# Kernel tuning notes

Measured on AMD Instinct MI355X. Metric: run time of the kernel, lower is better.

The kernel has to match this reference:

```python
import jax, jax.numpy as jnp
import numpy as np

D_MODEL = 256
D_INNER = 512
D_STATE = 16
DT_RANK = 16
D_CONV = 4


def setup_inputs() -> dict:
    key = jax.random.key(0)
    ks = jax.random.split(key, 10)
    f32 = jnp.float32
    x = jax.random.normal(ks[0], (8, D_MODEL, 128, 128), dtype=f32)
    W_in = jax.random.normal(ks[1], (D_MODEL, 2 * D_INNER), dtype=f32) * 0.02
    conv_w = jax.random.normal(ks[2], (D_INNER, D_CONV), dtype=f32) * 0.1
    conv_b = jnp.zeros((D_INNER,), dtype=f32)
    W_xproj = jax.random.normal(ks[3], (D_INNER, DT_RANK + 2 * D_STATE), dtype=f32) * 0.02
    W_dt = jax.random.normal(ks[4], (DT_RANK, D_INNER), dtype=f32) * 0.1
    b_dt = jax.random.normal(ks[5], (D_INNER,), dtype=f32) * 0.1
    # S4D-real init used by Mamba: A = -[1..d_state]
    A_log = jnp.log(jnp.broadcast_to(
        jnp.arange(1, D_STATE + 1, dtype=f32), (D_INNER, D_STATE))).copy()
    D = jnp.ones((D_INNER,), dtype=f32)
    W_out = jax.random.normal(ks[6], (D_INNER, D_MODEL), dtype=f32) * 0.02
    return {"x": x, "W_in": W_in, "conv_w": conv_w, "conv_b": conv_b,
            "W_xproj": W_xproj, "W_dt": W_dt, "b_dt": b_dt,
            "A_log": A_log, "D": D, "W_out": W_out}


def _mamba_l1(u, W_in, conv_w, conv_b, W_xproj, W_dt, b_dt, A_log, D, W_out):
    """Mamba block on N independent length-1 sequences. u: [N, d_model]."""
    dt_rank = W_dt.shape[0]
    d_state = A_log.shape[1]
    xz = u @ W_in                                   # [N, 2*d_inner]
    xi, z = jnp.split(xz, 2, axis=-1)               # each [N, d_inner]
    # Causal depthwise conv with left zero-padding; for L=1 only the last tap fires.
    xc = jax.nn.silu(xi * conv_w[:, -1] + conv_b)   # [N, d_inner]
    dbc = xc @ W_xproj                              # [N, dt_rank + 2*d_state]
    dt = dbc[:, :dt_rank]
    Bm = dbc[:, dt_rank:dt_rank + d_state]          # [N, d_state]
    Cm = dbc[:, dt_rank + d_state:]                 # [N, d_state]
    delta = jax.nn.softplus(dt @ W_dt + b_dt)       # [N, d_inner]
    # Single scan step from h0 = 0:
    #   h = exp(delta*A)*h0 + delta*B*u = delta*B*u  (A_log has zero effect/grad)
    #   y_d = sum_s h_{d,s} * C_s + D_d * u_d = delta_d*u_d*(B.C) + D_d*u_d
    bc = jnp.sum(Bm * Cm, axis=-1, keepdims=True)   # [N, 1]
    y = delta * xc * bc + D * xc                    # [N, d_inner]
    y = y * jax.nn.silu(z)
    return y @ W_out                                # [N, d_model]


def reference(x, W_in, conv_w, conv_b, W_xproj, W_dt, b_dt, A_log, D, W_out):
    B_, C, H, W = x.shape
    xs = x.transpose(0, 2, 3, 1).reshape(-1, C)     # [N, d_model], N = B*H*W
    y1 = _mamba_l1(xs, W_in, conv_w, conv_b, W_xproj, W_dt, b_dt, A_log, D, W_out)
    # torch.flip over a length-1 sequence dim is the identity -> y2 == y1
    y = (y1 + y1) * 0.5
    return y.reshape(B_, H, W, C).transpose(0, 3, 1, 2)
```

## Files before the change

kernel.cpp:

```cpp
#include <hip/hip_runtime.h>


typedef _Float16 f16x8 __attribute__((ext_vector_type(8)));
typedef _Float16 f16x2 __attribute__((ext_vector_type(2)));
typedef __fp16 fp16x2b __attribute__((ext_vector_type(2)));
typedef float f32x4 __attribute__((ext_vector_type(4)));

#define MFMA16(a,b,c) __builtin_amdgcn_mfma_f32_16x16x32_f16((a),(b),(c),0,0,0)

#define WPIN_OFF   0u
#define WPOUT_OFF  524288u
#define WPXP_OFF   786432u
#define WPDT_OFF   835584u

#define U_OFF     0
#define XC_OFF    0
#define DTP_OFF   65536
#define BC_OFF    69632
#define LDS_BYTES 69888

__device__ __forceinline__ unsigned short f16bits(float f) {
  union { _Float16 h; unsigned short u; } c; c.h = (_Float16)f; return c.u;
}
__device__ __forceinline__ unsigned pk2(float a, float b) {
  union { fp16x2b h; unsigned u; } c;
  c.h = __builtin_amdgcn_cvt_pkrtz(a, b);
  return c.u;
}
__device__ __forceinline__ f16x2 upk(unsigned u) {
  union { unsigned u; f16x2 h; } c; c.u = u; return c.h;
}
__device__ __forceinline__ float siluf(float t) {
  return t * __builtin_amdgcn_rcpf(1.f + __expf(-t));
}
__device__ __forceinline__ float softplusf(float t) {
  return fmaxf(t, 0.f) + __logf(1.f + __expf(-fabsf(t)));
}

__global__ void pack_w_kernel(const float* __restrict__ src,
                              unsigned short* __restrict__ dst,
                              int K, int N, int KB) {
  int t = blockIdx.x * 256 + threadIdx.x;
  if (t >= KB * N * 8) return;
  int ke = t & 7;
  int n  = (t >> 3) % N;
  int kb = t / (N * 8);
  int k  = kb * 8 + ke;
  float v = (k < K) ? src[k * N + n] : 0.f;
  dst[t] = f16bits(v);
}

__global__ void pack_win_kernel(const float* __restrict__ W_in,
                                const float* __restrict__ conv_w,
                                unsigned short* __restrict__ dst) {
  int t = blockIdx.x * 256 + threadIdx.x;
  int ke = t & 7;
  int n  = (t >> 3) & 1023;
  int kb = t >> 13;
  float v = W_in[(kb * 8 + ke) * 1024 + n];
  if (n < 512) v *= conv_w[n * 4 + 3];
  dst[t] = f16bits(v);
}

__global__ __launch_bounds__(512, 4) void mamba_fused_kernel(
    const float* __restrict__ x,
    const float* __restrict__ conv_b,
    const float* __restrict__ b_dt,
    const float* __restrict__ Dvec,
    float* __restrict__ out,
    const char* __restrict__ ws)
{
  __shared__ __align__(16) char smem[LDS_BYTES];

  const int tid  = threadIdx.x;
  const int wv   = tid >> 6;
  const int l    = tid & 63;
  const int lrow = l & 15;
  const int lhi  = l >> 4;

  const int wg   = blockIdx.x;
  const int w0   = (wg & 1) << 6;
  const int hb   = wg >> 1;
  const int h    = hb & 127;
  const int bidx = hb >> 7;

  const f16x8* wp_in  = (const f16x8*)(ws + WPIN_OFF);
  const f16x8* wp_out = (const f16x8*)(ws + WPOUT_OFF);
  const f16x8* wp_xp  = (const f16x8*)(ws + WPXP_OFF);
  const f16x8* wp_dt  = (const f16x8*)(ws + WPDT_OFF);

  if (tid < 128) {
    f32x4 z4 = {0.f, 0.f, 0.f, 0.f};
    *(f32x4*)(smem + DTP_OFF + 2048 + tid * 16) = z4;
  }

  {
    const float* xb = x + ((long)(bidx * 256) * 128 + h) * 128 + w0;
    #pragma unroll
    for (int i = 0; i < 4; ++i) {
      int cg = i * 8 + wv;
      float f[8];
      #pragma unroll
      for (int j = 0; j < 8; ++j)
        f[j] = __builtin_nontemporal_load(xb + (long)(cg * 8 + j) * 16384 + l);
      uint4 pk;
      pk.x = pk2(f[0], f[1]); pk.y = pk2(f[2], f[3]);
      pk.z = pk2(f[4], f[5]); pk.w = pk2(f[6], f[7]);
      *(uint4*)(smem + U_OFF + (cg * 64 + l) * 16) = pk;
    }
  }
  __syncthreads();

  unsigned xc_p[4][4][2];
  unsigned sz_p[4][4][2];

  #pragma unroll
  for (int hf = 0; hf < 2; ++hf) {
    const int cb = hf * 512 + wv * 64;
    #pragma unroll
    for (int rh = 0; rh < 2; ++rh) {
      f32x4 acc[4][2];
      #pragma unroll
      for (int q = 0; q < 4; ++q) {
        if (hf == 0) {
          f32x4 cb4 = *(const f32x4*)(conv_b + cb + q * 16 + lhi * 4);
          acc[q][0] = cb4; acc[q][1] = cb4;
        } else {
          f32x4 z4 = {0.f, 0.f, 0.f, 0.f};
          acc[q][0] = z4; acc[q][1] = z4;
        }
      }
      __builtin_amdgcn_s_setprio(1);
      #pragma unroll
      for (int s = 0; s < 8; ++s) {
        f16x8 b[2];
        #pragma unroll
        for (int r2 = 0; r2 < 2; ++r2)
          b[r2] = *(const f16x8*)(smem + U_OFF +
                    ((s * 4 + lhi) * 64 + (rh * 2 + r2) * 16 + lrow) * 16);
        f16x8 a[4];
        #pragma unroll
        for (int q = 0; q < 4; ++q)
          a[q] = wp_in[(s * 4 + lhi) * 1024 + cb + q * 16 + lrow];
        #pragma unroll
        for (int q = 0; q < 4; ++q)
          #pragma unroll
          for (int r2 = 0; r2 < 2; ++r2)
            acc[q][r2] = MFMA16(a[q], b[r2], acc[q][r2]);
      }
      __builtin_amdgcn_s_setprio(0);
      #pragma unroll
      for (int q = 0; q < 4; ++q) {
        #pragma unroll
        for (int r2 = 0; r2 < 2; ++r2) {
          const int rt = rh * 2 + r2;
          float s0 = siluf(acc[q][r2][0]);
          float s1 = siluf(acc[q][r2][1]);
          float s2 = siluf(acc[q][r2][2]);
          float s3 = siluf(acc[q][r2][3]);
          if (hf == 0) {
            xc_p[q][rt][0] = pk2(s0, s1); xc_p[q][rt][1] = pk2(s2, s3);
          } else {
            sz_p[q][rt][0] = pk2(s0, s1); sz_p[q][rt][1] = pk2(s2, s3);
          }
        }
      }
    }
  }
  __syncthreads();

  {
    #pragma unroll
    for (int q = 0; q < 4; ++q) {
      const int j0 = wv * 64 + q * 16 + lhi * 4;
      char* base = smem + XC_OFF + ((j0 >> 3) * 64) * 16 + (j0 & 7) * 2;
      #pragma unroll
      for (int rt = 0; rt < 4; ++rt) {
        uint2 w2; w2.x = xc_p[q][rt][0]; w2.y = xc_p[q][rt][1];
        *(uint2*)(base + (rt * 16 + lrow) * 16) = w2;
      }
    }
  }
  __syncthreads();

  {
    if (wv < 4) {
      const int mt = wv;
      f32x4 accB = {0.f,0.f,0.f,0.f}, accC = {0.f,0.f,0.f,0.f};
      #pragma unroll
      for (int s = 0; s < 16; ++s) {
        f16x8 bx = *(const f16x8*)(smem + XC_OFF + ((s * 4 + lhi) * 64 + mt * 16 + lrow) * 16);
        f16x8 aB = wp_xp[(s * 4 + lhi) * 48 + 16 + lrow];
        f16x8 aC = wp_xp[(s * 4 + lhi) * 48 + 32 + lrow];
        accB = MFMA16(aB, bx, accB);
        accC = MFMA16(aC, bx, accC);
      }
      float sbc = accB[0]*accC[0] + accB[1]*accC[1] + accB[2]*accC[2] + accB[3]*accC[3];
      sbc += __shfl_xor(sbc, 16);
      sbc += __shfl_xor(sbc, 32);
      if (lhi == 0)
        *(float*)(smem + BC_OFF + (mt * 16 + lrow) * 4) = sbc;
    } else {
      const int mt = wv - 4;
      f32x4 accD = {0.f,0.f,0.f,0.f};
      #pragma unroll
      for (int s = 0; s < 16; ++s) {
        f16x8 bx = *(const f16x8*)(smem + XC_OFF + ((s * 4 + lhi) * 64 + mt * 16 + lrow) * 16);
        f16x8 aD = wp_xp[(s * 4 + lhi) * 48 + lrow];
        accD = MFMA16(aD, bx, accD);
      }
      const int p0 = lhi * 4;
      uint2 w2; w2.x = pk2(accD[0], accD[1]); w2.y = pk2(accD[2], accD[3]);
      *(uint2*)(smem + DTP_OFF + ((p0 >> 3) * 64 + mt * 16 + lrow) * 16 + (p0 & 7) * 2) = w2;
    }
  }
  __syncthreads();

  {
    const int cb0 = wv * 64;
    f16x8 b3[4];
    #pragma unroll
    for (int rt = 0; rt < 4; ++rt)
      b3[rt] = *(const f16x8*)(smem + DTP_OFF + (lhi * 64 + rt * 16 + lrow) * 16);
    float bcr[4];
    #pragma unroll
    for (int rt = 0; rt < 4; ++rt)
      bcr[rt] = *(const float*)(smem + BC_OFF + (rt * 16 + lrow) * 4);
    #pragma unroll
    for (int q = 0; q < 4; ++q) {
      const int j0 = cb0 + q * 16 + lhi * 4;
      f32x4 bd = *(const f32x4*)(b_dt + j0);
      f32x4 dv = *(const f32x4*)(Dvec + j0);
      f16x8 a3 = wp_dt[lhi * 512 + cb0 + q * 16 + lrow];
      f32x4 acc3[4];
      #pragma unroll
      for (int rt = 0; rt < 4; ++rt)
        acc3[rt] = MFMA16(a3, b3[rt], bd);
      char* xbase = smem + XC_OFF + ((j0 >> 3) * 64) * 16 + (j0 & 7) * 2;
      #pragma unroll
      for (int rt = 0; rt < 4; ++rt) {
        uint2 yw;
        #pragma unroll
        for (int p = 0; p < 2; ++p) {
          f16x2 xv = upk(xc_p[q][rt][p]);
          f16x2 zv = upk(sz_p[q][rt][p]);
          f16x2 pr = xv * zv;
          float d0 = softplusf(acc3[rt][2 * p]);
          float d1 = softplusf(acc3[rt][2 * p + 1]);
          float y0 = (d0 * bcr[rt] + dv[2 * p])     * (float)pr[0];
          float y1 = (d1 * bcr[rt] + dv[2 * p + 1]) * (float)pr[1];
          unsigned u = pk2(y0, y1);
          if (p == 0) yw.x = u; else yw.y = u;
        }
        *(uint2*)(xbase + (rt * 16 + lrow) * 16) = yw;
      }
    }
  }
  __syncthreads();

  {
    f32x4 acc4[2][4];
    #pragma unroll
    for (int c2 = 0; c2 < 2; ++c2)
      #pragma unroll
      for (int mt = 0; mt < 4; ++mt) {
        f32x4 z4 = {0.f, 0.f, 0.f, 0.f};
        acc4[c2][mt] = z4;
      }
    __builtin_amdgcn_s_setprio(1);
    #pragma unroll
    for (int s = 0; s < 16; ++s) {
      f16x8 by[4];
      #pragma unroll
      for (int mt = 0; mt < 4; ++mt)
        by[mt] = *(const f16x8*)(smem + XC_OFF + ((s * 4 + lhi) * 64 + mt * 16 + lrow) * 16);
      f16x8 aw[2];
      #pragma unroll
      for (int c2 = 0; c2 < 2; ++c2)
        aw[c2] = wp_out[(s * 4 + lhi) * 256 + wv * 32 + c2 * 16 + lrow];
      #pragma unroll
      for (int c2 = 0; c2 < 2; ++c2)
        #pragma unroll
        for (int mt = 0; mt < 4; ++mt)
          acc4[c2][mt] = MFMA16(aw[c2], by[mt], acc4[c2][mt]);
    }
    __builtin_amdgcn_s_setprio(0);
    const long obase = (long)(bidx * 256 + wv * 32 + lhi * 4) * 16384 + h * 128 + w0 + lrow;
    #pragma unroll
    for (int c2 = 0; c2 < 2; ++c2)
      #pragma unroll
      for (int i = 0; i < 4; ++i)
        #pragma unroll
        for (int mt = 0; mt < 4; ++mt)
          __builtin_nontemporal_store(acc4[c2][mt][i],
              out + obase + (long)(c2 * 16 + i) * 16384 + mt * 16);
  }
}

extern "C" void kernel_launch(void* const* d_in, const int* in_sizes, int n_in,
                              void* d_out, int out_size, void* d_ws, size_t ws_size,
                              hipStream_t stream) {
  const float* x       = (const float*)d_in[0];
  const float* W_in    = (const float*)d_in[1];
  const float* conv_w  = (const float*)d_in[2];
  const float* conv_b  = (const float*)d_in[3];
  const float* W_xproj = (const float*)d_in[4];
  const float* W_dt    = (const float*)d_in[5];
  const float* b_dt    = (const float*)d_in[6];
  const float* Dvec    = (const float*)d_in[8];
  const float* W_out   = (const float*)d_in[9];
  float* out = (float*)d_out;
  char* ws = (char*)d_ws;

  pack_win_kernel<<<dim3(1024), dim3(256), 0, stream>>>(W_in, conv_w, (unsigned short*)(ws + WPIN_OFF));
  pack_w_kernel<<<dim3(512),  dim3(256), 0, stream>>>(W_out,   (unsigned short*)(ws + WPOUT_OFF), 512, 256, 64);
  pack_w_kernel<<<dim3(96),   dim3(256), 0, stream>>>(W_xproj, (unsigned short*)(ws + WPXP_OFF), 512, 48, 64);
  pack_w_kernel<<<dim3(64),   dim3(256), 0, stream>>>(W_dt,    (unsigned short*)(ws + WPDT_OFF), 16, 512, 4);

  mamba_fused_kernel<<<dim3(2048), dim3(512), 0, stream>>>(
      x, conv_b, b_dt, Dvec, out, (const char*)ws);
}
```

Baseline: 202.2 us.

## Switch fused Mamba kernel to 32x32x16 MFMA tiles across all GEMM stages

Replaces the 16x16x32 MFMA instructions with 32x32x16 ones in the input projection, dt projection and output projection, and remaps the LDS fragment layouts and output store indexing to match. The z-branch is computed first and kept in packed registers, while the x-branch accumulators are held in f32 until after the barrier. The dt-projection K padding shrinks from 32 to 16, which removes the zeroing of pad rows and shrinks LDS. Larger tiles cut operand loads per flop, but they need more accumulator registers, so launch bounds drop from 4 to 2 blocks per CU, which lowers occupancy.

```diff
diff --git a/kernel.cpp b/kernel.cpp
--- a/kernel.cpp
+++ b/kernel.cpp
@@ -5,8 +5,10 @@
 typedef _Float16 f16x2 __attribute__((ext_vector_type(2)));
 typedef __fp16 fp16x2b __attribute__((ext_vector_type(2)));
 typedef float f32x4 __attribute__((ext_vector_type(4)));
+typedef float f32x16 __attribute__((ext_vector_type(16)));
 
 #define MFMA16(a,b,c) __builtin_amdgcn_mfma_f32_16x16x32_f16((a),(b),(c),0,0,0)
+#define MFMA32(a,b,c) __builtin_amdgcn_mfma_f32_32x32x16_f16((a),(b),(c),0,0,0)
 
 #define WPIN_OFF   0u
 #define WPOUT_OFF  524288u
@@ -16,8 +18,8 @@
 #define U_OFF     0
 #define XC_OFF    0
 #define DTP_OFF   65536
-#define BC_OFF    69632
-#define LDS_BYTES 69888
+#define BC_OFF    67584
+#define LDS_BYTES 67840
 
 __device__ __forceinline__ unsigned short f16bits(float f) {
   union { _Float16 h; unsigned short u; } c; c.h = (_Float16)f; return c.u;
@@ -62,7 +64,7 @@
   dst[t] = f16bits(v);
 }
 
-__global__ __launch_bounds__(512, 4) void mamba_fused_kernel(
+__global__ __launch_bounds__(512, 2) void mamba_fused_kernel(
     const float* __restrict__ x,
     const float* __restrict__ conv_b,
     const float* __restrict__ b_dt,
@@ -77,6 +79,8 @@
   const int l    = tid & 63;
   const int lrow = l & 15;
   const int lhi  = l >> 4;
+  const int l31  = l & 31;
+  const int lh   = l >> 5;
 
   const int wg   = blockIdx.x;
   const int w0   = (wg & 1) << 6;
@@ -88,11 +92,6 @@
   const f16x8* wp_out = (const f16x8*)(ws + WPOUT_OFF);
   const f16x8* wp_xp  = (const f16x8*)(ws + WPXP_OFF);
   const f16x8* wp_dt  = (const f16x8*)(ws + WPDT_OFF);
-
-  if (tid < 128) {
-    f32x4 z4 = {0.f, 0.f, 0.f, 0.f};
-    *(f32x4*)(smem + DTP_OFF + 2048 + tid * 16) = z4;
-  }
 
   {
     const float* xb = x + ((long)(bidx * 256) * 128 + h) * 128 + w0;
@@ -111,74 +110,102 @@
   }
   __syncthreads();
 
-  unsigned xc_p[4][4][2];
-  unsigned sz_p[4][4][2];
-
-  #pragma unroll
-  for (int hf = 0; hf < 2; ++hf) {
-    const int cb = hf * 512 + wv * 64;
-    #pragma unroll
-    for (int rh = 0; rh < 2; ++rh) {
-      f32x4 acc[4][2];
-      #pragma unroll
-      for (int q = 0; q < 4; ++q) {
-        if (hf == 0) {
-          f32x4 cb4 = *(const f32x4*)(conv_b + cb + q * 16 + lhi * 4);
-          acc[q][0] = cb4; acc[q][1] = cb4;
-        } else {
-          f32x4 z4 = {0.f, 0.f, 0.f, 0.f};
-          acc[q][0] = z4; acc[q][1] = z4;
-        }
-      }
+  unsigned sz_pk[2][2][4][2];
+  f32x16 accx[2][2];
+
+  {
+    {
+      f32x16 acc[2][2];
+      #pragma unroll
+      for (int ct = 0; ct < 2; ++ct)
+        #pragma unroll
+        for (int rt = 0; rt < 2; ++rt)
+          #pragma unroll
+          for (int e = 0; e < 16; ++e) acc[ct][rt][e] = 0.f;
+      const int cb = 512 + wv * 64;
       __builtin_amdgcn_s_setprio(1);
       #pragma unroll
-      for (int s = 0; s < 8; ++s) {
+      for (int ks = 0; ks < 16; ++ks) {
         f16x8 b[2];
         #pragma unroll
-        for (int r2 = 0; r2 < 2; ++r2)
-          b[r2] = *(const f16x8*)(smem + U_OFF +
-                    ((s * 4 + lhi) * 64 + (rh * 2 + r2) * 16 + lrow) * 16);
-        f16x8 a[4];
-        #pragma unroll
-        for (int q = 0; q < 4; ++q)
-          a[q] = wp_in[(s * 4 + lhi) * 1024 + cb + q * 16 + lrow];
-        #pragma unroll
-        for (int q = 0; q < 4; ++q)
-          #pragma unroll
-          for (int r2 = 0; r2 < 2; ++r2)
-            acc[q][r2] = MFMA16(a[q], b[r2], acc[q][r2]);
+        for (int rt = 0; rt < 2; ++rt)
+          b[rt] = *(const f16x8*)(smem + U_OFF + ((2 * ks + lh) * 64 + rt * 32 + l31) * 16);
+        f16x8 a[2];
+        #pragma unroll
+        for (int ct = 0; ct < 2; ++ct)
+          a[ct] = wp_in[(2 * ks + lh) * 1024 + cb + ct * 32 + l31];
+        #pragma unroll
+        for (int ct = 0; ct < 2; ++ct)
+          #pragma unroll
+          for (int rt = 0; rt < 2; ++rt)
+            acc[ct][rt] = MFMA32(a[ct], b[rt], acc[ct][rt]);
       }
       __builtin_amdgcn_s_setprio(0);
       #pragma unroll
-      for (int q = 0; q < 4; ++q) {
-        #pragma unroll
-        for (int r2 = 0; r2 < 2; ++r2) {
-          const int rt = rh * 2 + r2;
-          float s0 = siluf(acc[q][r2][0]);
-          float s1 = siluf(acc[q][r2][1]);
-          float s2 = siluf(acc[q][r2][2]);
-          float s3 = siluf(acc[q][r2][3]);
-          if (hf == 0) {
-            xc_p[q][rt][0] = pk2(s0, s1); xc_p[q][rt][1] = pk2(s2, s3);
-          } else {
-            sz_p[q][rt][0] = pk2(s0, s1); sz_p[q][rt][1] = pk2(s2, s3);
+      for (int ct = 0; ct < 2; ++ct)
+        #pragma unroll
+        for (int rt = 0; rt < 2; ++rt)
+          #pragma unroll
+          for (int q4 = 0; q4 < 4; ++q4) {
+            float s0 = siluf(acc[ct][rt][4 * q4 + 0]);
+            float s1 = siluf(acc[ct][rt][4 * q4 + 1]);
+            float s2 = siluf(acc[ct][rt][4 * q4 + 2]);
+            float s3 = siluf(acc[ct][rt][4 * q4 + 3]);
+            sz_pk[ct][rt][q4][0] = pk2(s0, s1);
+            sz_pk[ct][rt][q4][1] = pk2(s2, s3);
+          }
+    }
+    {
+      const int cb = wv * 64;
+      #pragma unroll
+      for (int ct = 0; ct < 2; ++ct) {
+        #pragma unroll
+        for (int q4 = 0; q4 < 4; ++q4) {
+          f32x4 cb4 = *(const f32x4*)(conv_b + cb + ct * 32 + 8 * q4 + 4 * lh);
+          #pragma unroll
+          for (int i = 0; i < 4; ++i) {
+            accx[ct][0][4 * q4 + i] = cb4[i];
+            accx[ct][1][4 * q4 + i] = cb4[i];
           }
         }
       }
-    }
-  }
-  __syncthreads();
-
-  {
-    #pragma unroll
-    for (int q = 0; q < 4; ++q) {
-      const int j0 = wv * 64 + q * 16 + lhi * 4;
-      char* base = smem + XC_OFF + ((j0 >> 3) * 64) * 16 + (j0 & 7) * 2;
-      #pragma unroll
-      for (int rt = 0; rt < 4; ++rt) {
-        uint2 w2; w2.x = xc_p[q][rt][0]; w2.y = xc_p[q][rt][1];
-        *(uint2*)(base + (rt * 16 + lrow) * 16) = w2;
-      }
+      __builtin_amdgcn_s_setprio(1);
+      #pragma unroll
+      for (int ks = 0; ks < 16; ++ks) {
+        f16x8 b[2];
+        #pragma unroll
+        for (int rt = 0; rt < 2; ++rt)
+          b[rt] = *(const f16x8*)(smem + U_OFF + ((2 * ks + lh) * 64 + rt * 32 + l31) * 16);
+        f16x8 a[2];
+        #pragma unroll
+        for (int ct = 0; ct < 2; ++ct)
+          a[ct] = wp_in[(2 * ks + lh) * 1024 + cb + ct * 32 + l31];
+        #pragma unroll
+        for (int ct = 0; ct < 2; ++ct)
+          #pragma unroll
+          for (int rt = 0; rt < 2; ++rt)
+            accx[ct][rt] = MFMA32(a[ct], b[rt], accx[ct][rt]);
+      }
+      __builtin_amdgcn_s_setprio(0);
+    }
+  }
+  __syncthreads();
+
+  {
+    #pragma unroll
+    for (int ct = 0; ct < 2; ++ct) {
+      const int jb8 = (wv * 64 + ct * 32) >> 3;
+      #pragma unroll
+      for (int rt = 0; rt < 2; ++rt)
+        #pragma unroll
+        for (int q4 = 0; q4 < 4; ++q4) {
+          float s0 = siluf(accx[ct][rt][4 * q4 + 0]);
+          float s1 = siluf(accx[ct][rt][4 * q4 + 1]);
+          float s2 = siluf(accx[ct][rt][4 * q4 + 2]);
+          float s3 = siluf(accx[ct][rt][4 * q4 + 3]);
+          uint2 w2; w2.x = pk2(s0, s1); w2.y = pk2(s2, s3);
+          *(uint2*)(smem + XC_OFF + ((jb8 + q4) * 64 + rt * 32 + l31) * 16 + lh * 8) = w2;
+        }
     }
   }
   __syncthreads();
@@ -217,83 +244,82 @@
   __syncthreads();
 
   {
-    const int cb0 = wv * 64;
-    f16x8 b3[4];
-    #pragma unroll
-    for (int rt = 0; rt < 4; ++rt)
-      b3[rt] = *(const f16x8*)(smem + DTP_OFF + (lhi * 64 + rt * 16 + lrow) * 16);
-    float bcr[4];
-    #pragma unroll
-    for (int rt = 0; rt < 4; ++rt)
-      bcr[rt] = *(const float*)(smem + BC_OFF + (rt * 16 + lrow) * 4);
-    #pragma unroll
-    for (int q = 0; q < 4; ++q) {
-      const int j0 = cb0 + q * 16 + lhi * 4;
-      f32x4 bd = *(const f32x4*)(b_dt + j0);
-      f32x4 dv = *(const f32x4*)(Dvec + j0);
-      f16x8 a3 = wp_dt[lhi * 512 + cb0 + q * 16 + lrow];
-      f32x4 acc3[4];
-      #pragma unroll
-      for (int rt = 0; rt < 4; ++rt)
-        acc3[rt] = MFMA16(a3, b3[rt], bd);
-      char* xbase = smem + XC_OFF + ((j0 >> 3) * 64) * 16 + (j0 & 7) * 2;
-      #pragma unroll
-      for (int rt = 0; rt < 4; ++rt) {
-        uint2 yw;
-        #pragma unroll
-        for (int p = 0; p < 2; ++p) {
-          f16x2 xv = upk(xc_p[q][rt][p]);
-          f16x2 zv = upk(sz_p[q][rt][p]);
-          f16x2 pr = xv * zv;
-          float d0 = softplusf(acc3[rt][2 * p]);
-          float d1 = softplusf(acc3[rt][2 * p + 1]);
-          float y0 = (d0 * bcr[rt] + dv[2 * p])     * (float)pr[0];
-          float y1 = (d1 * bcr[rt] + dv[2 * p + 1]) * (float)pr[1];
-          unsigned u = pk2(y0, y1);
-          if (p == 0) yw.x = u; else yw.y = u;
+    f16x8 b3[2];
+    #pragma unroll
+    for (int rt = 0; rt < 2; ++rt)
+      b3[rt] = *(const f16x8*)(smem + DTP_OFF + (lh * 64 + rt * 32 + l31) * 16);
+    float bcm[2];
+    #pragma unroll
+    for (int rt = 0; rt < 2; ++rt)
+      bcm[rt] = *(const float*)(smem + BC_OFF + (rt * 32 + l31) * 4);
+    #pragma unroll
+    for (int ct = 0; ct < 2; ++ct) {
+      const int oc0 = wv * 64 + ct * 32;
+      f16x8 a3 = wp_dt[lh * 512 + oc0 + l31];
+      f32x16 cin;
+      f32x4 dv4[4];
+      #pragma unroll
+      for (int q4 = 0; q4 < 4; ++q4) {
+        f32x4 bd = *(const f32x4*)(b_dt + oc0 + 8 * q4 + 4 * lh);
+        #pragma unroll
+        for (int i = 0; i < 4; ++i) cin[4 * q4 + i] = bd[i];
+        dv4[q4] = *(const f32x4*)(Dvec + oc0 + 8 * q4 + 4 * lh);
+      }
+      #pragma unroll
+      for (int rt = 0; rt < 2; ++rt) {
+        f32x16 d = MFMA32(a3, b3[rt], cin);
+        #pragma unroll
+        for (int q4 = 0; q4 < 4; ++q4) {
+          char* xaddr = smem + XC_OFF + (((oc0 >> 3) + q4) * 64 + rt * 32 + l31) * 16 + lh * 8;
+          uint2 xcw = *(uint2*)xaddr;
+          uint2 yw;
+          #pragma unroll
+          for (int p = 0; p < 2; ++p) {
+            f16x2 xv = upk(p == 0 ? xcw.x : xcw.y);
+            f16x2 zv = upk(sz_pk[ct][rt][q4][p]);
+            f16x2 pr = xv * zv;
+            float d0 = softplusf(d[4 * q4 + 2 * p]);
+            float d1 = softplusf(d[4 * q4 + 2 * p + 1]);
+            float y0 = (d0 * bcm[rt] + dv4[q4][2 * p])     * (float)pr[0];
+            float y1 = (d1 * bcm[rt] + dv4[q4][2 * p + 1]) * (float)pr[1];
+            unsigned u = pk2(y0, y1);
+            if (p == 0) yw.x = u; else yw.y = u;
+          }
+          *(uint2*)xaddr = yw;
         }
-        *(uint2*)(xbase + (rt * 16 + lrow) * 16) = yw;
-      }
-    }
-  }
-  __syncthreads();
-
-  {
-    f32x4 acc4[2][4];
-    #pragma unroll
-    for (int c2 = 0; c2 < 2; ++c2)
-      #pragma unroll
-      for (int mt = 0; mt < 4; ++mt) {
-        f32x4 z4 = {0.f, 0.f, 0.f, 0.f};
-        acc4[c2][mt] = z4;
-      }
+      }
+    }
+  }
+  __syncthreads();
+
+  {
+    f32x16 acc4[2];
+    #pragma unroll
+    for (int rt = 0; rt < 2; ++rt)
+      #pragma unroll
+      for (int e = 0; e < 16; ++e) acc4[rt][e] = 0.f;
     __builtin_amdgcn_s_setprio(1);
     #pragma unroll
-    for (int s = 0; s < 16; ++s) {
-      f16x8 by[4];
-      #pragma unroll
-      for (int mt = 0; mt < 4; ++mt)
-        by[mt] = *(const f16x8*)(smem + XC_OFF + ((s * 4 + lhi) * 64 + mt * 16 + lrow) * 16);
-      f16x8 aw[2];
-      #pragma unroll
-      for (int c2 = 0; c2 < 2; ++c2)
-        aw[c2] = wp_out[(s * 4 + lhi) * 256 + wv * 32 + c2 * 16 + lrow];
-      #pragma unroll
-      for (int c2 = 0; c2 < 2; ++c2)
-        #pragma unroll
-        for (int mt = 0; mt < 4; ++mt)
-          acc4[c2][mt] = MFMA16(aw[c2], by[mt], acc4[c2][mt]);
+    for (int ks = 0; ks < 32; ++ks) {
+      f16x8 by[2];
+      #pragma unroll
+      for (int rt = 0; rt < 2; ++rt)
+        by[rt] = *(const f16x8*)(smem + XC_OFF + ((2 * ks + lh) * 64 + rt * 32 + l31) * 16);
+      f16x8 aw = wp_out[(2 * ks + lh) * 256 + wv * 32 + l31];
+      #pragma unroll
+      for (int rt = 0; rt < 2; ++rt)
+        acc4[rt] = MFMA32(aw, by[rt], acc4[rt]);
     }
     __builtin_amdgcn_s_setprio(0);
-    const long obase = (long)(bidx * 256 + wv * 32 + lhi * 4) * 16384 + h * 128 + w0 + lrow;
-    #pragma unroll
-    for (int c2 = 0; c2 < 2; ++c2)
-      #pragma unroll
-      for (int i = 0; i < 4; ++i)
-        #pragma unroll
-        for (int mt = 0; mt < 4; ++mt)
-          __builtin_nontemporal_store(acc4[c2][mt][i],
-              out + obase + (long)(c2 * 16 + i) * 16384 + mt * 16);
+    const long obase = (long)(bidx * 256 + wv * 32 + 4 * lh) * 16384 + h * 128 + w0 + l31;
+    #pragma unroll
+    for (int rt = 0; rt < 2; ++rt)
+      #pragma unroll
+      for (int q4 = 0; q4 < 4; ++q4)
+        #pragma unroll
+        for (int i = 0; i < 4; ++i)
+          __builtin_nontemporal_store(acc4[rt][4 * q4 + i],
+              out + obase + (long)(8 * q4 + i) * 16384 + rt * 32);
   }
 }
 
@@ -315,7 +341,7 @@
   pack_win_kernel<<<dim3(1024), dim3(256), 0, stream>>>(W_in, conv_w, (unsigned short*)(ws + WPIN_OFF));
   pack_w_kernel<<<dim3(512),  dim3(256), 0, stream>>>(W_out,   (unsigned short*)(ws + WPOUT_OFF), 512, 256, 64);
   pack_w_kernel<<<dim3(96),   dim3(256), 0, stream>>>(W_xproj, (unsigned short*)(ws + WPXP_OFF), 512, 48, 64);
-  pack_w_kernel<<<dim3(64),   dim3(256), 0, stream>>>(W_dt,    (unsigned short*)(ws + WPDT_OFF), 16, 512, 4);
+  pack_w_kernel<<<dim3(32),   dim3(256), 0, stream>>>(W_dt,    (unsigned short*)(ws + WPDT_OFF), 16, 512, 2);
 
   mamba_fused_kernel<<<dim3(2048), dim3(512), 0, stream>>>(
       x, conv_b, b_dt, Dvec, out, (const char*)ws);
```

New measurement: 227.5 us. 1.13x slower.
